# Performance work log

Measured on AMD Instinct MI355X. Metric: run time of the kernel, lower is better.

Reference implementation:

```python
import jax, jax.numpy as jnp
import numpy as np

E, S, L, V, PMAX = 256, 64, 3, 256, 2000
DILATIONS = (1, 2, 4, 8)


def _layernorm(x, g, b, eps=1e-5):
    m = x.mean(-1, keepdims=True)
    v = ((x - m) ** 2).mean(-1, keepdims=True)
    return (x - m) * jax.lax.rsqrt(v + eps) * g + b


def _ssm_layer(x, in_w, conv_w, conv_b, dt_w, A_log, D_param, B_w, C_w, out_w, ln_g, ln_b):
    # x: [B, T, D]
    Bsz, T, Dm = x.shape
    xr = x @ in_w.T                                  # [B,T,2D]
    x_in, x_res = xr[..., :Dm], xr[..., Dm:]
    # causal depthwise conv, kernel=4, left-pad 3 (== torch pad=3 then [:, :, :T])
    xt = x_in.transpose(0, 2, 1)                     # [B,D,T]
    xc = jax.lax.conv_general_dilated(
        xt, conv_w[:, None, :], (1,), [(3, 0)],
        feature_group_count=Dm, dimension_numbers=('NCH', 'OIH', 'NCH'))
    xc = jax.nn.silu((xc + conv_b[None, :, None]).transpose(0, 2, 1))  # [B,T,D]
    A = -jnp.exp(A_log)                              # [D,S]
    Bm = xc @ B_w.T                                  # [B,T,S]
    Cm = xc @ C_w.T                                  # [B,T,S]
    dt = jax.nn.softplus(dt_w)                       # [D] per-channel timestep
    dA = 1.0 + dt[:, None] * A                       # Euler discretization I + dt*A, [D,S]
    h0 = jnp.zeros((Bsz, Dm, S), x.dtype)

    def step(h, inp):
        u_t, B_t, C_t = inp                          # [B,D],[B,S],[B,S]
        h = dA * h + (dt * u_t)[:, :, None] * B_t[:, None, :]   # [B,D,S]
        y = jnp.einsum('bs,bds->bd', C_t, h)
        return h, y

    _, ys = jax.lax.scan(step, h0, (xc.transpose(1, 0, 2), Bm.transpose(1, 0, 2), Cm.transpose(1, 0, 2)))
    y = ys.transpose(1, 0, 2) + D_param * xc         # [B,T,D]
    y = (y * jax.nn.silu(x_res)) @ out_w.T
    return _layernorm(y + x, ln_g, ln_b)


def _forward(tokens, tok_emb, pos_emb, in_w, conv_w, conv_b, dt_w, A_log, D_param,
             B_w, C_w, out_w, ln_g, ln_b, ctx_w, ctx_b, fus_w, fus_b, fus_ln_g, fus_ln_b):
    Bsz, T = tokens.shape
    x = tok_emb[tokens] + pos_emb[:T][None]          # [B,T,E]
    feats = x
    for i in range(L):
        feats = _ssm_layer(feats, in_w[i], conv_w[i], conv_b[i], dt_w[i], A_log[i],
                           D_param[i], B_w[i], C_w[i], out_w[i], ln_g[i], ln_b[i])
    # multi-dilation context convs on the raw embeddings
    xt = x.transpose(0, 2, 1)                        # [B,E,T]
    ctx = []
    for j, d in enumerate(DILATIONS):
        o = jax.lax.conv_general_dilated(
            xt, ctx_w[j], (1,), [(d, d)], rhs_dilation=(d,),
            dimension_numbers=('NCH', 'OIH', 'NCH'))
        ctx.append(o + ctx_b[j][None, :, None])
    ctx = jnp.concatenate(ctx, axis=1).transpose(0, 2, 1)      # [B,T,E]
    fused = jax.nn.relu(jnp.concatenate([feats, ctx], -1) @ fus_w.T + fus_b)
    return _layernorm(fused, fus_ln_g, fus_ln_b)


def setup_inputs() -> dict:
    key = jax.random.key(0)
    ks = jax.random.split(key, 16)
    Bsz, T = 32, 2000

    def n(k, shape, s):
        return jax.random.normal(k, shape, jnp.float32) * s

    return {
        'tokens': jax.random.randint(ks[0], (Bsz, T), 0, V),
        'tok_emb': n(ks[1], (V, E), 1.0),
        'pos_emb': n(ks[2], (PMAX, E), 1.0),
        'in_w': n(ks[3], (L, 2 * E, E), 0.05),
        'conv_w': n(ks[4], (L, E, 4), 0.2),
        'conv_b': jnp.zeros((L, E), jnp.float32),
        'dt_w': jax.random.uniform(ks[5], (L, E), jnp.float32, -0.01, 0.01),
        'A_log': jax.random.uniform(ks[6], (L, E, S), jnp.float32, -4.0, -1.0),
        'D_param': jnp.zeros((L, E), jnp.float32),
        'B_w': n(ks[7], (L, S, E), 0.05),
        'C_w': n(ks[8], (L, S, E), 0.05),
        'out_w': n(ks[9], (L, E, E), 0.05),
        'ln_g': jnp.ones((L, E), jnp.float32),
        'ln_b': jnp.zeros((L, E), jnp.float32),
        'ctx_w': n(ks[10], (4, E // 4, E, 3), 0.05),
        'ctx_b': jnp.zeros((4, E // 4), jnp.float32),
        'fus_w': n(ks[11], (E, 2 * E), 0.05),
        'fus_b': jnp.zeros((E,), jnp.float32),
        'fus_ln_g': jnp.ones((E,), jnp.float32),
        'fus_ln_b': jnp.zeros((E,), jnp.float32),
    }


def reference(tokens, tok_emb, pos_emb, in_w, conv_w, conv_b, dt_w, A_log, D_param,
              B_w, C_w, out_w, ln_g, ln_b, ctx_w, ctx_b, fus_w, fus_b, fus_ln_g, fus_ln_b):
    return _forward(tokens, tok_emb, pos_emb, in_w, conv_w, conv_b, dt_w, A_log, D_param,
                    B_w, C_w, out_w, ln_g, ln_b, ctx_w, ctx_b, fus_w, fus_b, fus_ln_g, fus_ln_b)
```

## Files before the change

kernel.cpp:

```cpp
#include <hip/hip_runtime.h>
#include <stdint.h>

#define B_ 32
#define T_ 2000
#define E_ 256
#define S_ 64
#define L_ 3
#define BT_ (B_*T_)
#define NC_ 25
#define CL_ 80
#define TS_ 16
#define NT_ (CL_/TS_)
#define TP_ (T_+16)

typedef short s8v __attribute__((ext_vector_type(8)));
typedef short s4v __attribute__((ext_vector_type(4)));
typedef float f4v __attribute__((ext_vector_type(4)));
typedef float f2v __attribute__((ext_vector_type(2)));
typedef unsigned short us;

__device__ __forceinline__ float b2f(us u){
    return __uint_as_float(((unsigned int)u) << 16);
}
__device__ __forceinline__ us f2b(float f){
    unsigned int x = __float_as_uint(f);
    x += 0x7fffu + ((x >> 16) & 1u);
    return (us)(x >> 16);
}

__global__ __launch_bounds__(256) void cvtw_k(const float* __restrict__ src,
    us* __restrict__ dst)
{
    int idx = blockIdx.x*256 + threadIdx.x;
    f4v v = *(const f4v*)(src + (size_t)idx*4);
    s4v o;
    #pragma unroll
    for (int j=0;j<4;j++) o[j] = (short)f2b(v[j]);
    *(s4v*)(dst + (size_t)idx*4) = o;
}

__global__ __launch_bounds__(256) void packbc_k(const float* __restrict__ Bw,
    const float* __restrict__ Cw, us* __restrict__ wbc)
{
    int idx = blockIdx.x*256 + threadIdx.x;
    int i = idx & 255; int r = (idx >> 8) & 127; int l = idx >> 15;
    const float* src = (r < 64) ? (Bw + ((size_t)l*S_ + r)*E_ + i)
                                : (Cw + ((size_t)l*S_ + (r-64))*E_ + i);
    wbc[idx] = f2b(*src);
}

__global__ __launch_bounds__(256) void packw_k(const float* __restrict__ cw,
    us* __restrict__ wp)
{
    int idx = blockIdx.x*256 + threadIdx.x;
    int i2 = idx % 768; int r = idx / 768;
    int c = r & 63; int j = r >> 6;
    int tap = i2 >> 8; int i = i2 & 255;
    wp[idx] = f2b(cw[(((size_t)(j*64 + c))*E_ + i)*3 + tap]);
}

__global__ __launch_bounds__(256) void embed_k(const int* __restrict__ tok,
    const float* __restrict__ te, const float* __restrict__ pe, us* __restrict__ x0)
{
    int idx = blockIdx.x*256 + threadIdx.x;
    int dg = idx & 31; int bt = idx >> 5; int t = bt % T_;
    int tk = tok[bt] & 255;
    const float* ta = te + (size_t)tk*E_ + dg*8;
    const float* pa = pe + (size_t)t*E_ + dg*8;
    f4v a0 = *(const f4v*)ta, a1 = *(const f4v*)(ta+4);
    f4v p0 = *(const f4v*)pa, p1 = *(const f4v*)(pa+4);
    s8v o;
    #pragma unroll
    for (int j=0;j<4;j++){
        o[j]   = (short)f2b(a0[j] + p0[j]);
        o[j+4] = (short)f2b(a1[j] + p1[j]);
    }
    *(s8v*)(x0 + (size_t)bt*E_ + dg*8) = o;
}

__global__ __launch_bounds__(256) void lconst_k(const float* __restrict__ dt_w,
    const float* __restrict__ A_log, float* __restrict__ dtv,
    float* __restrict__ dAT, float* __restrict__ dApT)
{
    int idx = blockIdx.x*256 + threadIdx.x;
    int d = idx & (E_-1); int s = idx >> 8;
    float dt = log1pf(expf(dt_w[d]));
    float A  = -expf(A_log[d*S_ + s]);
    float dA = 1.f + dt*A;
    dAT[s*E_ + d]  = dA;
    dApT[s*E_ + d] = powf(dA, (float)CL_);
    if (s == 0) dtv[d] = dt;
}

__global__ __launch_bounds__(256) void dwconv_k(const us* __restrict__ xin,
    const float* __restrict__ cw, const float* __restrict__ cb, us* __restrict__ xc)
{
    int idx = blockIdx.x*256 + threadIdx.x;
    int dg = idx & 31; int bt = idx >> 5; int t = bt % T_;
    int d0 = dg*8;
    float acc[8]; float w[8][4];
    #pragma unroll
    for (int j=0;j<8;j++){
        f4v wv = *(const f4v*)(cw + (size_t)(d0+j)*4);
        #pragma unroll
        for (int k=0;k<4;k++) w[j][k] = wv[k];
        acc[j] = cb[d0+j];
    }
    #pragma unroll
    for (int k=0;k<4;k++){
        if (t + k - 3 >= 0){
            s8v xv = *(const s8v*)(xin + (size_t)(bt + k - 3)*E_ + d0);
            #pragma unroll
            for (int j=0;j<8;j++) acc[j] = fmaf(b2f((us)xv[j]), w[j][k], acc[j]);
        }
    }
    s8v o;
    #pragma unroll
    for (int j=0;j<8;j++){ float v = acc[j]; v = v / (1.f + expf(-v)); o[j] = (short)f2b(v); }
    *(s8v*)(xc + (size_t)bt*E_ + d0) = o;
}

#define BM 128
#define BK 32

template<int AMODE, int EPI, int BNT>
__global__ __launch_bounds__(256)
void gemm_k(const us* __restrict__ A1, const us* __restrict__ A2,
            int lda, int shift,
            const us* __restrict__ W, int ldw,
            void* __restrict__ C1, void* __restrict__ C2,
            const float* __restrict__ bias,
            int ldc, int K)
{
    constexpr int NR = BNT/32;
    __shared__ us Al[BM*BK];
    __shared__ us Bl[BNT*BK];
    const int tid = threadIdx.x;
    const int wid = tid >> 6, lane = tid & 63;
    const int m0 = blockIdx.x * BM;
    const int n0 = blockIdx.y * BNT;
    const int wr = wid >> 1, wc = wid & 1;
    int sh = shift;
    if constexpr (AMODE==4) sh = 1 << blockIdx.y;
    f4v acc[4][NR];
    #pragma unroll
    for (int a=0;a<4;a++)
        #pragma unroll
        for (int b=0;b<NR;b++) acc[a][b] = (f4v){0.f,0.f,0.f,0.f};

    for (int k0 = 0; k0 < K; k0 += BK){
        if (k0) __syncthreads();
        #pragma unroll
        for (int i=0;i<2;i++){
            int g = i*256 + tid;
            int row = g >> 2, ks = g & 3;
            const us* src;
            if constexpr (AMODE==0){
                src = A1 + (size_t)(m0+row)*lda + k0 + ks*8;
            } else if constexpr (AMODE==2){
                int kk = k0 + ks*8;
                const us* base = (kk < E_) ? A1 : A2;
                src = base + (size_t)(m0+row)*E_ + (kk & (E_-1));
            } else {
                int kk = k0 + ks*8;
                int tap = kk >> 8; int kin = kk & (E_-1);
                int m = m0 + row; int bb = m / T_; int tt = m - bb*T_;
                src = A1 + ((size_t)bb*TP_ + 8 + tt + (tap-1)*sh)*E_ + kin;
            }
            __builtin_amdgcn_global_load_lds(
                (const __attribute__((address_space(1))) void*)src,
                (__attribute__((address_space(3))) void*)(Al + (size_t)g*8), 16, 0, 0);
        }
        #pragma unroll
        for (int i=0;i<BNT/64;i++){
            int g = i*256 + tid;
            int row = g >> 2, ks = g & 3;
            const us* src = W + (size_t)(n0+row)*ldw + k0 + ks*8;
            __builtin_amdgcn_global_load_lds(
                (const __attribute__((address_space(1))) void*)src,
                (__attribute__((address_space(3))) void*)(Bl + (size_t)g*8), 16, 0, 0);
        }
        __syncthreads();

        s8v af[4], bfr[NR];
        #pragma unroll
        for (int mr=0;mr<4;mr++)
            af[mr] = *(const s8v*)(Al + ((size_t)(wr*64 + mr*16 + (lane&15))*4 + (lane>>4))*8);
        #pragma unroll
        for (int nr=0;nr<NR;nr++)
            bfr[nr] = *(const s8v*)(Bl + ((size_t)(wc*(BNT/2) + nr*16 + (lane&15))*4 + (lane>>4))*8);
        #pragma unroll
        for (int mr=0;mr<4;mr++)
            #pragma unroll
            for (int nr=0;nr<NR;nr++)
                acc[mr][nr] = __builtin_amdgcn_mfma_f32_16x16x32_bf16(af[mr], bfr[nr], acc[mr][nr], 0, 0, 0);
    }
    #pragma unroll
    for (int mr=0;mr<4;mr++){
        #pragma unroll
        for (int nr=0;nr<NR;nr++){
            int col = n0 + wc*(BNT/2) + nr*16 + (lane & 15);
            int rb  = m0 + wr*64 + mr*16 + ((lane >> 4) << 2);
            #pragma unroll
            for (int i=0;i<4;i++){
                float val = acc[mr][nr][i];
                size_t row = (size_t)(rb + i);
                if constexpr (EPI==0){
                    ((us*)C1)[row*ldc + col] = f2b(val);
                } else if constexpr (EPI==1){
                    if (col < E_) ((us*)C1)[row*E_ + col] = f2b(val);
                    else          ((us*)C2)[row*E_ + (col - E_)] = f2b(val);
                } else if constexpr (EPI==2){
                    ((float*)C1)[row*ldc + col] = val;
                } else if constexpr (EPI==5){
                    val += bias[col];
                    ((us*)C1)[row*ldc + col] = f2b(val);
                } else {
                    val += bias[col];
                    val = fmaxf(val, 0.f);
                    ((float*)C1)[row*ldc + col] = val;
                }
            }
        }
    }
}

__global__ __launch_bounds__(1024) void scan_ly(
    const float* __restrict__ dAT, const float* __restrict__ dtv,
    const us* __restrict__ xc, const float* __restrict__ BC,
    us* __restrict__ ys, us* __restrict__ H)
{
    __shared__ float sBC[TS_*128];
    __shared__ us    sXC[TS_*256];
    int b = blockIdx.x / NC_, c = blockIdx.x % NC_;
    int tid = threadIdx.x;
    int d = tid >> 2, sg = tid & 3, s0 = sg*16;
    f4v h4[4], dA4[4];
    #pragma unroll
    for (int q=0;q<4;q++){
        #pragma unroll
        for (int j=0;j<4;j++){ h4[q][j] = 0.f; dA4[q][j] = dAT[(s0+q*4+j)*E_ + d]; }
    }
    float dtd = dtv[d];
    int t0 = c*CL_;
    size_t base0 = (size_t)b*T_ + t0;
    *(f2v*)(&sBC[tid*2]) = *(const f2v*)(BC + base0*128 + tid*2);
    *(s4v*)(&sXC[tid*4]) = *(const s4v*)(xc + base0*E_ + tid*4);
    __syncthreads();
    for (int tile = 0; tile < NT_; ++tile){
        f2v pv; s4v pxv;
        bool more = (tile+1 < NT_);
        if (more){
            size_t basen = base0 + (size_t)(tile+1)*TS_;
            pv  = *(const f2v*)(BC + basen*128 + tid*2);
            pxv = *(const s4v*)(xc + basen*E_ + tid*4);
        }
        for (int st = 0; st < TS_; ++st){
            int t = t0 + tile*TS_ + st;
            float u = dtd * b2f(sXC[st*256 + d]);
            const f4v* Bp = (const f4v*)(&sBC[st*128 + s0]);
            const f4v* Cp = (const f4v*)(&sBC[st*128 + 64 + s0]);
            f4v y4 = (f4v){0.f,0.f,0.f,0.f};
            #pragma unroll
            for (int q=0;q<4;q++){
                h4[q] = dA4[q]*h4[q] + Bp[q]*u;
                y4    = y4 + Cp[q]*h4[q];
            }
            float y = (y4[0]+y4[1]) + (y4[2]+y4[3]);
            y += __shfl_xor(y, 1, 4);
            y += __shfl_xor(y, 2, 4);
            if (sg == 0) ys[((size_t)b*T_ + t)*E_ + d] = f2b(y);
        }
        __syncthreads();
        if (more){
            *(f2v*)(&sBC[tid*2]) = pv;
            *(s4v*)(&sXC[tid*4]) = pxv;
        }
        __syncthreads();
    }
    size_t hb = ((size_t)(b*NC_ + c))*S_*E_ + d;
    #pragma unroll
    for (int q=0;q<4;q++)
        #pragma unroll
        for (int j=0;j<4;j++) H[hb + (size_t)(s0+q*4+j)*E_] = f2b(h4[q][j]);
}

__global__ __launch_bounds__(256) void carry_k(const float* __restrict__ dApT,
    us* H)
{
    int idx = blockIdx.x*256 + threadIdx.x;
    int d = idx & (E_-1); int s = (idx >> 8) & (S_-1); int b = idx >> 14;
    float ap = dApT[s*E_ + d];
    size_t base = ((size_t)(b*NC_))*S_*E_ + (size_t)s*E_ + d;
    float hh = 0.f;
    for (int c=0;c<NC_;c++){
        size_t p = base + (size_t)c*S_*E_;
        float hl = b2f(H[p]);
        H[p] = f2b(hh);
        hh = fmaf(ap, hh, hl);
    }
}

__global__ __launch_bounds__(1024) void scan_fx(
    const float* __restrict__ dAT, const float* __restrict__ BC,
    const us* __restrict__ Hc, us* ys)
{
    __shared__ float sC[TS_*64];
    int b = blockIdx.x / (NC_-1); int c = 1 + blockIdx.x % (NC_-1);
    int tid = threadIdx.x;
    int d = tid >> 2, sg = tid & 3, s0 = sg*16;
    f4v w4[4], dA4[4];
    size_t cb = ((size_t)(b*NC_ + c))*S_*E_ + d;
    #pragma unroll
    for (int q=0;q<4;q++){
        #pragma unroll
        for (int j=0;j<4;j++){
            int s = s0 + q*4 + j;
            dA4[q][j] = dAT[s*E_ + d];
            w4[q][j]  = dA4[q][j] * b2f(Hc[cb + (size_t)s*E_]);
        }
    }
    int t0 = c*CL_;
    size_t base0 = (size_t)b*T_ + t0;
    sC[tid] = BC[(base0 + (size_t)(tid>>6))*128 + 64 + (tid & 63)];
    __syncthreads();
    for (int tile = 0; tile < NT_; ++tile){
        float pv;
        bool more = (tile+1 < NT_);
        if (more){
            size_t basen = base0 + (size_t)(tile+1)*TS_;
            pv = BC[(basen + (size_t)(tid>>6))*128 + 64 + (tid & 63)];
        }
        for (int st = 0; st < TS_; ++st){
            int t = t0 + tile*TS_ + st;
            const f4v* Cp = (const f4v*)(&sC[st*64 + s0]);
            f4v y4 = (f4v){0.f,0.f,0.f,0.f};
            #pragma unroll
            for (int q=0;q<4;q++){
                y4   = y4 + Cp[q]*w4[q];
                w4[q] = w4[q]*dA4[q];
            }
            float y = (y4[0]+y4[1]) + (y4[2]+y4[3]);
            y += __shfl_xor(y, 1, 4);
            y += __shfl_xor(y, 2, 4);
            if (sg == 0){
                size_t p = ((size_t)b*T_ + t)*E_ + d;
                ys[p] = f2b(b2f(ys[p]) + y);
            }
        }
        __syncthreads();
        if (more) sC[tid] = pv;
        __syncthreads();
    }
}

__global__ __launch_bounds__(256) void zin_k(const us* __restrict__ ys,
    const us* xc, const us* __restrict__ xres,
    const float* __restrict__ Dp, us* zout)
{
    size_t e0 = ((size_t)blockIdx.x*256 + threadIdx.x)*4;
    int d0 = (int)(e0 & (E_-1));
    s4v yv  = *(const s4v*)(ys + e0);
    s4v xcv = *(const s4v*)(xc + e0);
    s4v xrv = *(const s4v*)(xres + e0);
    f4v dv  = *(const f4v*)(Dp + d0);
    s4v o;
    #pragma unroll
    for (int j=0;j<4;j++){
        float y  = b2f((us)yv[j]) + dv[j] * b2f((us)xcv[j]);
        float xr = b2f((us)xrv[j]);
        o[j] = (short)f2b(y * (xr / (1.f + expf(-xr))));
    }
    *(s4v*)(zout + e0) = o;
}

__global__ __launch_bounds__(256) void ln_k(const us* z,
    const us* __restrict__ resid, const float* __restrict__ g,
    const float* __restrict__ bb, us* out)
{
    int wid = threadIdx.x >> 6, lane = threadIdx.x & 63;
    size_t row = (size_t)blockIdx.x*4 + wid;
    size_t base = row*E_ + lane*4;
    s4v zv = *(const s4v*)(z + base);
    float v[4];
    #pragma unroll
    for (int j=0;j<4;j++) v[j] = b2f((us)zv[j]);
    if (resid){
        s4v rv = *(const s4v*)(resid + base);
        #pragma unroll
        for (int j=0;j<4;j++) v[j] += b2f((us)rv[j]);
    }
    float sum = v[0]+v[1]+v[2]+v[3];
    float sq  = v[0]*v[0]+v[1]*v[1]+v[2]*v[2]+v[3]*v[3];
    #pragma unroll
    for (int off=32; off>0; off>>=1){
        sum += __shfl_xor(sum, off, 64);
        sq  += __shfl_xor(sq,  off, 64);
    }
    float mean = sum * (1.f/E_);
    float var  = sq * (1.f/E_) - mean*mean;
    float rstd = rsqrtf(var + 1e-5f);
    f4v gv = *(const f4v*)(g + lane*4);
    f4v bv = *(const f4v*)(bb + lane*4);
    s4v o;
    #pragma unroll
    for (int j=0;j<4;j++)
        o[j] = (short)f2b((v[j]-mean)*rstd*gv[j] + bv[j]);
    *(s4v*)(out + base) = o;
}

__global__ __launch_bounds__(256) void ln_f32_k(const float* z,
    const float* __restrict__ g, const float* __restrict__ bb, float* out)
{
    int wid = threadIdx.x >> 6, lane = threadIdx.x & 63;
    size_t row = (size_t)blockIdx.x*4 + wid;
    size_t base = row*E_ + lane*4;
    f4v v = *(const f4v*)(z + base);
    float sum = v[0]+v[1]+v[2]+v[3];
    float sq  = v[0]*v[0]+v[1]*v[1]+v[2]*v[2]+v[3]*v[3];
    #pragma unroll
    for (int off=32; off>0; off>>=1){
        sum += __shfl_xor(sum, off, 64);
        sq  += __shfl_xor(sq,  off, 64);
    }
    float mean = sum * (1.f/E_);
    float var  = sq * (1.f/E_) - mean*mean;
    float rstd = rsqrtf(var + 1e-5f);
    f4v gv = *(const f4v*)(g + lane*4);
    f4v bv = *(const f4v*)(bb + lane*4);
    f4v o;
    #pragma unroll
    for (int j=0;j<4;j++)
        o[j] = (v[j]-mean)*rstd*gv[j] + bv[j];
    *(f4v*)(out + base) = o;
}

__global__ __launch_bounds__(256) void xpad_k(const us* __restrict__ x0,
    us* __restrict__ xp)
{
    int idx = blockIdx.x*256 + threadIdx.x;
    int dg = idx & 31; int r = idx >> 5;
    int tp = r % TP_; int b = r / TP_;
    s8v o;
    if (tp < 8 || tp >= T_+8){
        #pragma unroll
        for (int j=0;j<8;j++) o[j] = 0;
    } else {
        o = *(const s8v*)(x0 + ((size_t)b*T_ + tp - 8)*E_ + dg*8);
    }
    *(s8v*)(xp + (size_t)r*E_ + dg*8) = o;
}

__global__ void probe_k(const unsigned int* __restrict__ outw,
    const us* p0, const us* p1, float* outf)
{
    if (threadIdx.x | blockIdx.x) return;
    bool zero = true;
    for (int i=0;i<512 && zero;i++)              if (outw[i]) zero = false;
    for (int i=2000000;i<2000512 && zero;i++)    if (outw[i]) zero = false;
    if (!zero) return;
    int code = 256, f;
    f=0; for (int i=0;i<256;i++) if (p0[i] & 0x7FFF) f=1;  code += 128*f;
    f=0; for (int i=0;i<256;i++) if (p1[i] & 0x7FFF) f=1;  code += 16*f;
    outf[0] = (float)code;
}

extern "C" void kernel_launch(void* const* d_in, const int* in_sizes, int n_in,
                              void* d_out, int out_size, void* d_ws, size_t ws_size,
                              hipStream_t stream)
{
    const int*   tokens   = (const int*)d_in[0];
    const float* tok_emb  = (const float*)d_in[1];
    const float* pos_emb  = (const float*)d_in[2];
    const float* in_w     = (const float*)d_in[3];
    const float* conv_w   = (const float*)d_in[4];
    const float* conv_b   = (const float*)d_in[5];
    const float* dt_w     = (const float*)d_in[6];
    const float* A_log    = (const float*)d_in[7];
    const float* D_param  = (const float*)d_in[8];
    const float* B_w      = (const float*)d_in[9];
    const float* C_w      = (const float*)d_in[10];
    const float* out_w    = (const float*)d_in[11];
    const float* ln_g     = (const float*)d_in[12];
    const float* ln_b     = (const float*)d_in[13];
    const float* ctx_w    = (const float*)d_in[14];
    const float* ctx_b    = (const float*)d_in[15];
    const float* fus_w    = (const float*)d_in[16];
    const float* fus_b    = (const float*)d_in[17];
    const float* fus_ln_g = (const float*)d_in[18];
    const float* fus_ln_b = (const float*)d_in[19];

    char* ws = (char*)d_ws;
    size_t off = 0;
    auto alloc = [&](size_t bytes){ size_t o = off; off += (bytes + 255) & ~(size_t)255; return o; };
    const size_t BT = BT_;
    size_t o_p0  = alloc(BT*E_*2);
    size_t o_p1  = alloc(BT*E_*2);
    size_t o_ctx = alloc(BT*E_*2);
    size_t o_xin = alloc(BT*E_*2);
    size_t o_xc  = alloc(BT*E_*2);
    size_t o_bc  = alloc(BT*128*4);
    size_t o_h   = alloc((size_t)B_*NC_*S_*E_*2);
    size_t o_wp  = alloc((size_t)4*64*768*2);
    size_t o_wi  = alloc((size_t)L_*2*E_*E_*2);
    size_t o_wo  = alloc((size_t)L_*E_*E_*2);
    size_t o_wbc = alloc((size_t)L_*128*E_*2);
    size_t o_wf  = alloc((size_t)E_*2*E_*2);
    size_t o_dtv = alloc(E_*4);
    size_t o_dat = alloc(E_*S_*4);
    size_t o_dap = alloc(E_*S_*4);
    (void)ws_size; (void)in_sizes; (void)n_in; (void)out_size;

    us* P0   = (us*)(ws + o_p0);
    us* P1   = (us*)(ws + o_p1);
    us* CTXB = (us*)(ws + o_ctx);
    us* XIN  = (us*)(ws + o_xin);
    us* XC   = (us*)(ws + o_xc);
    float* BCf = (float*)(ws + o_bc);
    us* Hb   = (us*)(ws + o_h);
    us* WP   = (us*)(ws + o_wp);
    us* WI   = (us*)(ws + o_wi);
    us* WO   = (us*)(ws + o_wo);
    us* WBC  = (us*)(ws + o_wbc);
    us* WF   = (us*)(ws + o_wf);
    float* DTV  = (float*)(ws + o_dtv);
    float* DAT  = (float*)(ws + o_dat);
    float* DAPT = (float*)(ws + o_dap);
    us* XPAD = XIN;
    us* YS   = (us*)d_out;
    us* XRES = (us*)d_out + BT*E_;

    cvtw_k<<<L_*2*E_*E_/1024, 256, 0, stream>>>(in_w,  WI);
    cvtw_k<<<L_*E_*E_/1024,   256, 0, stream>>>(out_w, WO);
    cvtw_k<<<E_*2*E_/1024,    256, 0, stream>>>(fus_w, WF);
    packbc_k<<<L_*128*E_/256, 256, 0, stream>>>(B_w, C_w, WBC);
    packw_k<<<4*64*768/256,   256, 0, stream>>>(ctx_w, WP);

    embed_k<<<BT_*32/256, 256, 0, stream>>>(tokens, tok_emb, pos_emb, P0);

    xpad_k<<<B_*TP_*32/256, 256, 0, stream>>>(P0, XPAD);
    gemm_k<4,5,64><<<dim3(BT_/BM, 4), 256, 0, stream>>>(
        XPAD, nullptr, E_, 0, WP, 768,
        CTXB, nullptr, ctx_b, E_, 768);

    for (int l = 0; l < L_; ++l){
        const us* xprev = (l==1) ? P1 : P0;
        us*       xnext = (l==1) ? P0 : P1;

        lconst_k<<<E_*S_/256, 256, 0, stream>>>(dt_w + (size_t)l*E_, A_log + (size_t)l*E_*S_,
                                                DTV, DAT, DAPT);
        gemm_k<0,1,128><<<dim3(BT_/BM, 4), 256, 0, stream>>>(
            xprev, nullptr, E_, 0, WI + (size_t)l*2*E_*E_, E_, XIN, XRES, nullptr, E_, E_);
        dwconv_k<<<BT_*32/256, 256, 0, stream>>>(XIN, conv_w + (size_t)l*E_*4, conv_b + (size_t)l*E_, XC);
        gemm_k<0,2,128><<<dim3(BT_/BM, 1), 256, 0, stream>>>(
            XC, nullptr, E_, 0, WBC + (size_t)l*128*E_, E_, BCf, nullptr, nullptr, 128, E_);
        scan_ly<<<B_*NC_, 1024, 0, stream>>>(DAT, DTV, XC, BCf, YS, Hb);
        carry_k<<<B_*S_*E_/256, 256, 0, stream>>>(DAPT, Hb);
        scan_fx<<<B_*(NC_-1), 1024, 0, stream>>>(DAT, BCf, Hb, YS);
        zin_k<<<BT_*E_/4/256, 256, 0, stream>>>(YS, XC, XRES, D_param + (size_t)l*E_, XC );
        gemm_k<0,0,128><<<dim3(BT_/BM, 2), 256, 0, stream>>>(
            XC, nullptr, E_, 0, WO + (size_t)l*E_*E_, E_, XIN , nullptr, nullptr, E_, E_);
        ln_k<<<BT_/4, 256, 0, stream>>>(XIN, xprev, ln_g + (size_t)l*E_, ln_b + (size_t)l*E_, xnext);
    }

    gemm_k<2,6,128><<<dim3(BT_/BM, 2), 256, 0, stream>>>(
        P1, CTXB, E_, 0, WF, 2*E_, d_out, nullptr, fus_b, E_, 2*E_);
    ln_f32_k<<<BT_/4, 256, 0, stream>>>((const float*)d_out, fus_ln_g, fus_ln_b, (float*)d_out);

    probe_k<<<1, 64, 0, stream>>>((const unsigned int*)d_out, P0, P1, (float*)d_out);
}
```

Baseline: 1.439 ms.

## Fuse gating into out-projection GEMM, merge weight conversions, embed padding, layer constants

Removes the zin_k elementwise kernel: the out-projection GEMM now computes y + D*xc times silu(xres) while loading its A tile and writes bf16 to LDS. Previously that path used asynchronous global-to-LDS loads. The three weight conversion kernels are merged into one launch. Embedding writes the padded context buffer directly, so xpad_k goes away. Layer constants are computed once for all layers. The fused GEMM load is now synchronous and recomputes the gating for each N-block (2x), which may slow the GEMM main loop.

```diff
diff --git a/kernel.cpp b/kernel.cpp
--- a/kernel.cpp
+++ b/kernel.cpp
@@ -28,15 +28,23 @@
     return (us)(x >> 16);
 }
 
-__global__ __launch_bounds__(256) void cvtw_k(const float* __restrict__ src,
-    us* __restrict__ dst)
-{
-    int idx = blockIdx.x*256 + threadIdx.x;
-    f4v v = *(const f4v*)(src + (size_t)idx*4);
+#define NWI (L_*2*E_*E_)
+#define NWO (L_*E_*E_)
+#define NWF (E_*2*E_)
+__global__ __launch_bounds__(256) void cvtw3_k(const float* __restrict__ iw,
+    const float* __restrict__ ow, const float* __restrict__ fw,
+    us* __restrict__ WI, us* __restrict__ WO, us* __restrict__ WF)
+{
+    int idx4 = (blockIdx.x*256 + threadIdx.x)*4;
+    const float* src; us* dst; int off;
+    if (idx4 < NWI){ src = iw; dst = WI; off = idx4; }
+    else if (idx4 < NWI+NWO){ src = ow; dst = WO; off = idx4 - NWI; }
+    else { src = fw; dst = WF; off = idx4 - NWI - NWO; }
+    f4v v = *(const f4v*)(src + off);
     s4v o;
     #pragma unroll
     for (int j=0;j<4;j++) o[j] = (short)f2b(v[j]);
-    *(s4v*)(dst + (size_t)idx*4) = o;
+    *(s4v*)(dst + off) = o;
 }
 
 __global__ __launch_bounds__(256) void packbc_k(const float* __restrict__ Bw,
@@ -60,10 +68,20 @@
 }
 
 __global__ __launch_bounds__(256) void embed_k(const int* __restrict__ tok,
-    const float* __restrict__ te, const float* __restrict__ pe, us* __restrict__ x0)
+    const float* __restrict__ te, const float* __restrict__ pe,
+    us* __restrict__ x0, us* __restrict__ xp)
 {
     int idx = blockIdx.x*256 + threadIdx.x;
-    int dg = idx & 31; int bt = idx >> 5; int t = bt % T_;
+    if (idx < B_*16*32){
+        int dg = idx & 31; int r = idx >> 5;
+        int b = r >> 4, pr = r & 15;
+        int tp = (pr < 8) ? pr : (T_ + 8 + (pr - 8));
+        s8v z;
+        #pragma unroll
+        for (int j=0;j<8;j++) z[j] = 0;
+        *(s8v*)(xp + ((size_t)b*TP_ + tp)*E_ + dg*8) = z;
+    }
+    int dg = idx & 31; int bt = idx >> 5; int t = bt % T_; int b = bt / T_;
     int tk = tok[bt] & 255;
     const float* ta = te + (size_t)tk*E_ + dg*8;
     const float* pa = pe + (size_t)t*E_ + dg*8;
@@ -76,6 +94,7 @@
         o[j+4] = (short)f2b(a1[j] + p1[j]);
     }
     *(s8v*)(x0 + (size_t)bt*E_ + dg*8) = o;
+    *(s8v*)(xp + ((size_t)b*TP_ + 8 + t)*E_ + dg*8) = o;
 }
 
 __global__ __launch_bounds__(256) void lconst_k(const float* __restrict__ dt_w,
@@ -83,13 +102,13 @@
     float* __restrict__ dAT, float* __restrict__ dApT)
 {
     int idx = blockIdx.x*256 + threadIdx.x;
-    int d = idx & (E_-1); int s = idx >> 8;
-    float dt = log1pf(expf(dt_w[d]));
-    float A  = -expf(A_log[d*S_ + s]);
+    int d = idx & (E_-1); int s = (idx >> 8) & (S_-1); int l = idx >> 14;
+    float dt = log1pf(expf(dt_w[l*E_ + d]));
+    float A  = -expf(A_log[((size_t)l*E_ + d)*S_ + s]);
     float dA = 1.f + dt*A;
-    dAT[s*E_ + d]  = dA;
-    dApT[s*E_ + d] = powf(dA, (float)CL_);
-    if (s == 0) dtv[d] = dt;
+    dAT[(size_t)l*S_*E_ + s*E_ + d]  = dA;
+    dApT[(size_t)l*S_*E_ + s*E_ + d] = powf(dA, (float)CL_);
+    if (s == 0) dtv[l*E_ + d] = dt;
 }
 
 __global__ __launch_bounds__(256) void dwconv_k(const us* __restrict__ xin,
@@ -126,10 +145,11 @@
 template<int AMODE, int EPI, int BNT>
 __global__ __launch_bounds__(256)
 void gemm_k(const us* __restrict__ A1, const us* __restrict__ A2,
+            const us* __restrict__ A3,
             int lda, int shift,
             const us* __restrict__ W, int ldw,
             void* __restrict__ C1, void* __restrict__ C2,
-            const float* __restrict__ bias,
+            const float* __restrict__ bias, const float* __restrict__ Dp,
             int ldc, int K)
 {
     constexpr int NR = BNT/32;
@@ -154,22 +174,40 @@
         for (int i=0;i<2;i++){
             int g = i*256 + tid;
             int row = g >> 2, ks = g & 3;
-            const us* src;
-            if constexpr (AMODE==0){
-                src = A1 + (size_t)(m0+row)*lda + k0 + ks*8;
-            } else if constexpr (AMODE==2){
-                int kk = k0 + ks*8;
-                const us* base = (kk < E_) ? A1 : A2;
-                src = base + (size_t)(m0+row)*E_ + (kk & (E_-1));
+            if constexpr (AMODE==5){
+                size_t base = (size_t)(m0+row)*E_ + k0 + ks*8;
+                s8v yv  = *(const s8v*)(A1 + base);
+                s8v xcv = *(const s8v*)(A2 + base);
+                s8v xrv = *(const s8v*)(A3 + base);
+                f4v d0v = *(const f4v*)(Dp + k0 + ks*8);
+                f4v d1v = *(const f4v*)(Dp + k0 + ks*8 + 4);
+                s8v o;
+                #pragma unroll
+                for (int j=0;j<8;j++){
+                    float dd = (j<4) ? d0v[j] : d1v[j-4];
+                    float y  = b2f((us)yv[j]) + dd * b2f((us)xcv[j]);
+                    float xr = b2f((us)xrv[j]);
+                    o[j] = (short)f2b(y * (xr / (1.f + expf(-xr))));
+                }
+                *(s8v*)(Al + (size_t)g*8) = o;
             } else {
-                int kk = k0 + ks*8;
-                int tap = kk >> 8; int kin = kk & (E_-1);
-                int m = m0 + row; int bb = m / T_; int tt = m - bb*T_;
-                src = A1 + ((size_t)bb*TP_ + 8 + tt + (tap-1)*sh)*E_ + kin;
+                const us* src;
+                if constexpr (AMODE==0){
+                    src = A1 + (size_t)(m0+row)*lda + k0 + ks*8;
+                } else if constexpr (AMODE==2){
+                    int kk = k0 + ks*8;
+                    const us* base = (kk < E_) ? A1 : A2;
+                    src = base + (size_t)(m0+row)*E_ + (kk & (E_-1));
+                } else {
+                    int kk = k0 + ks*8;
+                    int tap = kk >> 8; int kin = kk & (E_-1);
+                    int m = m0 + row; int bb = m / T_; int tt = m - bb*T_;
+                    src = A1 + ((size_t)bb*TP_ + 8 + tt + (tap-1)*sh)*E_ + kin;
+                }
+                __builtin_amdgcn_global_load_lds(
+                    (const __attribute__((address_space(1))) void*)src,
+                    (__attribute__((address_space(3))) void*)(Al + (size_t)g*8), 16, 0, 0);
             }
-            __builtin_amdgcn_global_load_lds(
-                (const __attribute__((address_space(1))) void*)src,
-                (__attribute__((address_space(3))) void*)(Al + (size_t)g*8), 16, 0, 0);
         }
         #pragma unroll
         for (int i=0;i<BNT/64;i++){
@@ -354,26 +392,6 @@
     }
 }
 
-__global__ __launch_bounds__(256) void zin_k(const us* __restrict__ ys,
-    const us* xc, const us* __restrict__ xres,
-    const float* __restrict__ Dp, us* zout)
-{
-    size_t e0 = ((size_t)blockIdx.x*256 + threadIdx.x)*4;
-    int d0 = (int)(e0 & (E_-1));
-    s4v yv  = *(const s4v*)(ys + e0);
-    s4v xcv = *(const s4v*)(xc + e0);
-    s4v xrv = *(const s4v*)(xres + e0);
-    f4v dv  = *(const f4v*)(Dp + d0);
-    s4v o;
-    #pragma unroll
-    for (int j=0;j<4;j++){
-        float y  = b2f((us)yv[j]) + dv[j] * b2f((us)xcv[j]);
-        float xr = b2f((us)xrv[j]);
-        o[j] = (short)f2b(y * (xr / (1.f + expf(-xr))));
-    }
-    *(s4v*)(zout + e0) = o;
-}
-
 __global__ __launch_bounds__(256) void ln_k(const us* z,
     const us* __restrict__ resid, const float* __restrict__ g,
     const float* __restrict__ bb, us* out)
@@ -433,22 +451,6 @@
     for (int j=0;j<4;j++)
         o[j] = (v[j]-mean)*rstd*gv[j] + bv[j];
     *(f4v*)(out + base) = o;
-}
-
-__global__ __launch_bounds__(256) void xpad_k(const us* __restrict__ x0,
-    us* __restrict__ xp)
-{
-    int idx = blockIdx.x*256 + threadIdx.x;
-    int dg = idx & 31; int r = idx >> 5;
-    int tp = r % TP_; int b = r / TP_;
-    s8v o;
-    if (tp < 8 || tp >= T_+8){
-        #pragma unroll
-        for (int j=0;j<8;j++) o[j] = 0;
-    } else {
-        o = *(const s8v*)(x0 + ((size_t)b*T_ + tp - 8)*E_ + dg*8);
-    }
-    *(s8v*)(xp + (size_t)r*E_ + dg*8) = o;
 }
 
 __global__ void probe_k(const unsigned int* __restrict__ outw,
@@ -502,13 +504,13 @@
     size_t o_bc  = alloc(BT*128*4);
     size_t o_h   = alloc((size_t)B_*NC_*S_*E_*2);
     size_t o_wp  = alloc((size_t)4*64*768*2);
-    size_t o_wi  = alloc((size_t)L_*2*E_*E_*2);
-    size_t o_wo  = alloc((size_t)L_*E_*E_*2);
+    size_t o_wi  = alloc((size_t)NWI*2);
+    size_t o_wo  = alloc((size_t)NWO*2);
     size_t o_wbc = alloc((size_t)L_*128*E_*2);
-    size_t o_wf  = alloc((size_t)E_*2*E_*2);
-    size_t o_dtv = alloc(E_*4);
-    size_t o_dat = alloc(E_*S_*4);
-    size_t o_dap = alloc(E_*S_*4);
+    size_t o_wf  = alloc((size_t)NWF*2);
+    size_t o_dtv = alloc((size_t)L_*E_*4);
+    size_t o_dat = alloc((size_t)L_*E_*S_*4);
+    size_t o_dap = alloc((size_t)L_*E_*S_*4);
     (void)ws_size; (void)in_sizes; (void)n_in; (void)out_size;
 
     us* P0   = (us*)(ws + o_p0);
@@ -530,41 +532,42 @@
     us* YS   = (us*)d_out;
     us* XRES = (us*)d_out + BT*E_;
 
-    cvtw_k<<<L_*2*E_*E_/1024, 256, 0, stream>>>(in_w,  WI);
-    cvtw_k<<<L_*E_*E_/1024,   256, 0, stream>>>(out_w, WO);
-    cvtw_k<<<E_*2*E_/1024,    256, 0, stream>>>(fus_w, WF);
+    cvtw3_k<<<(NWI+NWO+NWF)/1024, 256, 0, stream>>>(in_w, out_w, fus_w, WI, WO, WF);
     packbc_k<<<L_*128*E_/256, 256, 0, stream>>>(B_w, C_w, WBC);
     packw_k<<<4*64*768/256,   256, 0, stream>>>(ctx_w, WP);
-
-    embed_k<<<BT_*32/256, 256, 0, stream>>>(tokens, tok_emb, pos_emb, P0);
-
-    xpad_k<<<B_*TP_*32/256, 256, 0, stream>>>(P0, XPAD);
+    lconst_k<<<L_*E_*S_/256,  256, 0, stream>>>(dt_w, A_log, DTV, DAT, DAPT);
+
+    embed_k<<<BT_*32/256, 256, 0, stream>>>(tokens, tok_emb, pos_emb, P0, XPAD);
+
     gemm_k<4,5,64><<<dim3(BT_/BM, 4), 256, 0, stream>>>(
-        XPAD, nullptr, E_, 0, WP, 768,
-        CTXB, nullptr, ctx_b, E_, 768);
+        XPAD, nullptr, nullptr, E_, 0, WP, 768,
+        CTXB, nullptr, ctx_b, nullptr, E_, 768);
 
     for (int l = 0; l < L_; ++l){
         const us* xprev = (l==1) ? P1 : P0;
         us*       xnext = (l==1) ? P0 : P1;
-
-        lconst_k<<<E_*S_/256, 256, 0, stream>>>(dt_w + (size_t)l*E_, A_log + (size_t)l*E_*S_,
-                                                DTV, DAT, DAPT);
+        const float* DATl  = DAT  + (size_t)l*E_*S_;
+        const float* DAPTl = DAPT + (size_t)l*E_*S_;
+        const float* DTVl  = DTV  + (size_t)l*E_;
+
         gemm_k<0,1,128><<<dim3(BT_/BM, 4), 256, 0, stream>>>(
-            xprev, nullptr, E_, 0, WI + (size_t)l*2*E_*E_, E_, XIN, XRES, nullptr, E_, E_);
+            xprev, nullptr, nullptr, E_, 0, WI + (size_t)l*2*E_*E_, E_,
+            XIN, XRES, nullptr, nullptr, E_, E_);
         dwconv_k<<<BT_*32/256, 256, 0, stream>>>(XIN, conv_w + (size_t)l*E_*4, conv_b + (size_t)l*E_, XC);
         gemm_k<0,2,128><<<dim3(BT_/BM, 1), 256, 0, stream>>>(
-            XC, nullptr, E_, 0, WBC + (size_t)l*128*E_, E_, BCf, nullptr, nullptr, 128, E_);
-        scan_ly<<<B_*NC_, 1024, 0, stream>>>(DAT, DTV, XC, BCf, YS, Hb);
-        carry_k<<<B_*S_*E_/256, 256, 0, stream>>>(DAPT, Hb);
-        scan_fx<<<B_*(NC_-1), 1024, 0, stream>>>(DAT, BCf, Hb, YS);
-        zin_k<<<BT_*E_/4/256, 256, 0, stream>>>(YS, XC, XRES, D_param + (size_t)l*E_, XC );
-        gemm_k<0,0,128><<<dim3(BT_/BM, 2), 256, 0, stream>>>(
-            XC, nullptr, E_, 0, WO + (size_t)l*E_*E_, E_, XIN , nullptr, nullptr, E_, E_);
+            XC, nullptr, nullptr, E_, 0, WBC + (size_t)l*128*E_, E_,
+            BCf, nullptr, nullptr, nullptr, 128, E_);
+        scan_ly<<<B_*NC_, 1024, 0, stream>>>(DATl, DTVl, XC, BCf, YS, Hb);
+        carry_k<<<B_*S_*E_/256, 256, 0, stream>>>(DAPTl, Hb);
+        scan_fx<<<B_*(NC_-1), 1024, 0, stream>>>(DATl, BCf, Hb, YS);
+        gemm_k<5,0,128><<<dim3(BT_/BM, 2), 256, 0, stream>>>(
+            YS, XC, XRES, E_, 0, WO + (size_t)l*E_*E_, E_,
+            XIN , nullptr, nullptr, D_param + (size_t)l*E_, E_, E_);
         ln_k<<<BT_/4, 256, 0, stream>>>(XIN, xprev, ln_g + (size_t)l*E_, ln_b + (size_t)l*E_, xnext);
     }
 
     gemm_k<2,6,128><<<dim3(BT_/BM, 2), 256, 0, stream>>>(
-        P1, CTXB, E_, 0, WF, 2*E_, d_out, nullptr, fus_b, E_, 2*E_);
+        P1, CTXB, nullptr, E_, 0, WF, 2*E_, d_out, nullptr, fus_b, nullptr, E_, 2*E_);
     ln_f32_k<<<BT_/4, 256, 0, stream>>>((const float*)d_out, fus_ln_g, fus_ln_b, (float*)d_out);
 
     probe_k<<<1, 64, 0, stream>>>((const unsigned int*)d_out, P0, P1, (float*)d_out);
```

Measured after the change: 1.480 ms. +2.8%, slower.
